# Performance work log

Hardware: AMD Instinct MI355X
Metric: run time of the kernel (lower is better)

The kernel has to match this reference:

```python
import jax, jax.numpy as jnp
import numpy as np

D = 4096        # hidden_dim / latent_dim
R = 512         # number of latents
H = 32          # n_heads
HD = D // H     # head_dim = 128
T = 8192        # total tokens (sum of seqlens)
EPS = 1e-5


def layernorm(x, w, b):
    mu = jnp.mean(x, axis=-1, keepdims=True)
    var = jnp.mean(jnp.square(x - mu), axis=-1, keepdims=True)
    return (x - mu) * jax.lax.rsqrt(var + EPS) * w + b


def setup_inputs() -> dict:
    key = jax.random.key(0)
    ks = jax.random.split(key, 16)
    s = 0.02
    inp = {
        'x': jax.random.normal(ks[0], (T, D), jnp.float32),
        'seqlens': jnp.full((8,), T // 8, jnp.int64) if False else jnp.full((8,), T // 8, jnp.int32),
        'latents': jax.random.normal(ks[1], (R, D), jnp.float32),
        # PreNorm layernorms (query norm on x, context norm on latents)
        'ln_q_w': 1.0 + 0.1 * jax.random.normal(ks[2], (D,), jnp.float32),
        'ln_q_b': 0.1 * jax.random.normal(ks[3], (D,), jnp.float32),
        'ln_c_w': 1.0 + 0.1 * jax.random.normal(ks[4], (D,), jnp.float32),
        'ln_c_b': 0.1 * jax.random.normal(ks[5], (D,), jnp.float32),
        # attention projections, stored (in, out) so y = x @ W
        'Wq': s * jax.random.normal(ks[6], (D, D), jnp.float32),
        'Wk': s * jax.random.normal(ks[7], (D, D), jnp.float32),
        'Wv': s * jax.random.normal(ks[8], (D, D), jnp.float32),
        'Wo': s * jax.random.normal(ks[9], (D, D), jnp.float32),
        # single PreNorm MLP block (n_layers=1)
        'ln_m_w': 1.0 + 0.1 * jax.random.normal(ks[10], (D,), jnp.float32),
        'ln_m_b': 0.1 * jax.random.normal(ks[11], (D,), jnp.float32),
        'W1': s * jax.random.normal(ks[12], (D, D), jnp.float32),
        'W2': s * jax.random.normal(ks[13], (D, D), jnp.float32),
    }
    return inp


def reference(x, seqlens, latents, ln_q_w, ln_q_b, ln_c_w, ln_c_b,
              Wq, Wk, Wv, Wo, ln_m_w, ln_m_b, W1, W2):
    # --- PreNorm cross-attention: queries = ragged tokens, KV = latents ---
    # BlockDiagonalMask(q_seqlen=seqlens, kv_seqlen=[r]*b) with identical
    # latents per block == dense attention of all tokens vs the r latents.
    xq = layernorm(x, ln_q_w, ln_q_b)                 # (T, D)
    xc = layernorm(latents, ln_c_w, ln_c_b)           # (R, D)
    q = (xq @ Wq).reshape(T, H, HD)                   # (T, H, HD)
    k = (xc @ Wk).reshape(R, H, HD)                   # (R, H, HD)
    v = (xc @ Wv).reshape(R, H, HD)
    scale = HD ** -0.5
    scores = jnp.einsum('thd,rhd->htr', q, k) * scale  # (H, T, R)
    attn = jax.nn.softmax(scores, axis=-1)
    o = jnp.einsum('htr,rhd->thd', attn, v).reshape(T, D)
    attn_out = o @ Wo                                  # (T, D)

    hiddens = attn_out + x                             # residual

    # --- PreNorm MLP block (n_layers=1) ---
    y = layernorm(hiddens, ln_m_w, ln_m_b)
    m = jax.nn.gelu(y @ W1, approximate=False) @ W2 + y  # MLP_block inner residual
    hiddens = m + hiddens                                # outer residual

    # compress_rate == -1 -> mean_mask is None, output passes through
    return hiddens
```

## Files before the change

### kernel.cpp

```cpp
#include <hip/hip_runtime.h>
#include <hip/hip_bf16.h>
#include <math.h>

#define D 4096
#define T 8192
#define R 512
#define HD 128
#define NH 32

typedef unsigned short u16;
typedef u16 u16x8 __attribute__((ext_vector_type(8)));
typedef __bf16 bf16x8 __attribute__((ext_vector_type(8)));
typedef float f32x4 __attribute__((ext_vector_type(4)));

__device__ __forceinline__ u16 f2bf(float f) {
  unsigned u = __builtin_bit_cast(unsigned, f);
  u += 0x7FFFu + ((u >> 16) & 1u);
  return (u16)(u >> 16);
}
__device__ __forceinline__ float bf2f(u16 b) {
  return __builtin_bit_cast(float, ((unsigned)b) << 16);
}
__device__ __forceinline__ bf16x8 ldb8(const u16* p) {
  return __builtin_bit_cast(bf16x8, *(const u16x8*)p);
}
__device__ __forceinline__ void async_cp16(void* gsrc, void* ldst) {
  typedef __attribute__((address_space(1))) void gvoid;
  typedef __attribute__((address_space(3))) void lvoid;
  __builtin_amdgcn_global_load_lds((gvoid*)gsrc, (lvoid*)ldst, 16, 0, 0);
}
#define MFMA(a, b, c) __builtin_amdgcn_mfma_f32_16x16x32_bf16(a, b, c, 0, 0, 0)

__global__ __launch_bounds__(256) void ln_bf16(
    const float* __restrict__ X, const float* __restrict__ w,
    const float* __restrict__ b, u16* __restrict__ out) {
  const int row = blockIdx.x, tid = threadIdx.x;
  const int lane = tid & 63, wv = tid >> 6;
  const float* xr = X + (long)row * D;
  float4 v[4];
  float s = 0.f, ss = 0.f;
#pragma unroll
  for (int i = 0; i < 4; ++i) {
    v[i] = *(const float4*)(xr + tid * 4 + i * 1024);
    s += v[i].x + v[i].y + v[i].z + v[i].w;
    ss += v[i].x * v[i].x + v[i].y * v[i].y + v[i].z * v[i].z + v[i].w * v[i].w;
  }
#pragma unroll
  for (int off = 32; off >= 1; off >>= 1) {
    s += __shfl_xor(s, off);
    ss += __shfl_xor(ss, off);
  }
  __shared__ float sw[4], ssw[4];
  if (lane == 0) { sw[wv] = s; ssw[wv] = ss; }
  __syncthreads();
  s = sw[0] + sw[1] + sw[2] + sw[3];
  ss = ssw[0] + ssw[1] + ssw[2] + ssw[3];
  const float mu = s * (1.f / D);
  const float var = ss * (1.f / D) - mu * mu;
  const float rstd = rsqrtf(var + 1e-5f);
#pragma unroll
  for (int i = 0; i < 4; ++i) {
    const int base = tid * 4 + i * 1024;
    const float4 wv4 = *(const float4*)(w + base);
    const float4 bv4 = *(const float4*)(b + base);
    ushort4 ov;
    ov.x = f2bf((v[i].x - mu) * rstd * wv4.x + bv4.x);
    ov.y = f2bf((v[i].y - mu) * rstd * wv4.y + bv4.y);
    ov.z = f2bf((v[i].z - mu) * rstd * wv4.z + bv4.z);
    ov.w = f2bf((v[i].w - mu) * rstd * wv4.w + bv4.w);
    *(ushort4*)(out + (long)row * D + base) = ov;
  }
}

__global__ __launch_bounds__(256) void wconv(const float* __restrict__ W,
                                             u16* __restrict__ Wt) {
  __shared__ float t[32][33];
  const int tx = threadIdx.x & 31, ty = threadIdx.x >> 5;
  const int n0 = blockIdx.x * 32, k0 = blockIdx.y * 32;
#pragma unroll
  for (int i = 0; i < 4; ++i)
    t[ty + i * 8][tx] = W[(long)(k0 + ty + i * 8) * D + n0 + tx];
  __syncthreads();
#pragma unroll
  for (int i = 0; i < 4; ++i)
    Wt[(long)(n0 + ty + i * 8) * D + k0 + tx] = f2bf(t[tx][ty + i * 8]);
}

template <int EPI>
__global__ __launch_bounds__(256) void gemm_bt(
    const u16* __restrict__ A, const u16* __restrict__ Bt, u16* __restrict__ ob,
    u16* __restrict__ ob2, float* __restrict__ of, const float* __restrict__ af,
    const u16* __restrict__ ab, float scale) {
  __shared__ u16 As[128 * 32];
  __shared__ u16 Bs[128 * 32];
  const int tid = threadIdx.x;
  const int bx = blockIdx.x, by = blockIdx.y;
  const int lane = tid & 63, w = tid >> 6;
  const int ln15 = lane & 15, q = lane >> 4;
  const int wm = (w >> 1) * 64, wn = (w & 1) * 64;

  const int c0 = tid, c1 = tid + 256;
  const u16* ag0 = A + (long)(by * 128 + (c0 >> 2)) * D + (c0 & 3) * 8;
  const u16* ag1 = A + (long)(by * 128 + (c1 >> 2)) * D + (c1 & 3) * 8;
  const u16* bg0 = Bt + (long)(bx * 128 + (c0 >> 2)) * D + (c0 & 3) * 8;
  const u16* bg1 = Bt + (long)(bx * 128 + (c1 >> 2)) * D + (c1 & 3) * 8;
  u16* al0 = As + (tid & ~63) * 8;
  u16* al1 = As + ((tid & ~63) + 256) * 8;
  u16* bl0 = Bs + (tid & ~63) * 8;
  u16* bl1 = Bs + ((tid & ~63) + 256) * 8;

  f32x4 acc[4][4];
#pragma unroll
  for (int i = 0; i < 4; ++i)
#pragma unroll
    for (int j = 0; j < 4; ++j) {
      f32x4 z = {0.f, 0.f, 0.f, 0.f};
      acc[i][j] = z;
    }

  for (int k0 = 0; k0 < D; k0 += 32) {
    __syncthreads();
    async_cp16((void*)(ag0 + k0), al0);
    async_cp16((void*)(ag1 + k0), al1);
    async_cp16((void*)(bg0 + k0), bl0);
    async_cp16((void*)(bg1 + k0), bl1);
    __syncthreads();
    bf16x8 av[4], bv[4];
#pragma unroll
    for (int i = 0; i < 4; ++i) av[i] = ldb8(As + (wm + i * 16 + ln15) * 32 + q * 8);
#pragma unroll
    for (int j = 0; j < 4; ++j) bv[j] = ldb8(Bs + (wn + j * 16 + ln15) * 32 + q * 8);
#pragma unroll
    for (int i = 0; i < 4; ++i)
#pragma unroll
      for (int j = 0; j < 4; ++j) acc[i][j] = MFMA(av[i], bv[j], acc[i][j]);
  }

#pragma unroll
  for (int i = 0; i < 4; ++i) {
    const int gmb = by * 128 + wm + i * 16 + q * 4;
#pragma unroll
    for (int j = 0; j < 4; ++j) {
      const int gn = bx * 128 + wn + j * 16 + ln15;
#pragma unroll
      for (int r = 0; r < 4; ++r) {
        const int gm = gmb + r;
        const float vacc = acc[i][j][r];
        const long idx = (long)gm * D + gn;
        if constexpr (EPI == 0) {
          ob[idx] = f2bf(vacc * scale);
        } else if constexpr (EPI == 1) {
          if (gn < D)
            ob[idx] = f2bf(vacc);
          else
            ob2[(long)(gn - D) * R + gm] = f2bf(vacc);
        } else if constexpr (EPI == 2) {
          of[idx] = vacc + af[idx];
        } else if constexpr (EPI == 3) {
          ob[idx] = f2bf(0.5f * vacc * (1.f + erff(vacc * 0.7071067811865475f)));
        } else {
          of[idx] = of[idx] + vacc + bf2f(ab[idx]);
        }
      }
    }
  }
}

__global__ __launch_bounds__(256) void attn_fused(const u16* Q,
                                                  const u16* __restrict__ Kb,
                                                  const u16* __restrict__ Vt,
                                                  u16* O) {
  __shared__ u16 Qs[64 * 136];
  __shared__ u16 Ks[64 * 136];
  __shared__ u16 Vs[128 * 72];
  __shared__ u16 Ps[4][16 * 72];
  const int tid = threadIdx.x;
  const int lane = tid & 63, w = tid >> 6;
  const int ln15 = lane & 15, q = lane >> 4;
  const int t0 = blockIdx.x * 64, h = blockIdx.y;

#pragma unroll
  for (int it = 0; it < 4; ++it) {
    const int c = tid + it * 256;
    const int row = c >> 4, cj = c & 15;
    *(u16x8*)(Qs + row * 136 + cj * 8) =
        *(const u16x8*)(Q + (long)(t0 + row) * D + h * HD + cj * 8);
  }

  f32x4 o[8];
  float m_run[4], l_run[4];
#pragma unroll
  for (int t = 0; t < 8; ++t) {
    f32x4 z = {0.f, 0.f, 0.f, 0.f};
    o[t] = z;
  }
#pragma unroll
  for (int r = 0; r < 4; ++r) {
    m_run[r] = -1e30f;
    l_run[r] = 0.f;
  }

  for (int ch = 0; ch < 8; ++ch) {
    const int r0 = ch * 64;
    __syncthreads();
#pragma unroll
    for (int it = 0; it < 4; ++it) {
      const int c = tid + it * 256;
      const int row = c >> 4, cj = c & 15;
      *(u16x8*)(Ks + row * 136 + cj * 8) =
          *(const u16x8*)(Kb + (long)(r0 + row) * D + h * HD + cj * 8);
    }
#pragma unroll
    for (int it = 0; it < 4; ++it) {
      const int c = tid + it * 256;
      const int hd = c >> 3, rj = c & 7;
      *(u16x8*)(Vs + hd * 72 + rj * 8) =
          *(const u16x8*)(Vt + (long)(h * HD + hd) * R + r0 + rj * 8);
    }
    __syncthreads();

    f32x4 s[4];
#pragma unroll
    for (int j = 0; j < 4; ++j) {
      f32x4 z = {0.f, 0.f, 0.f, 0.f};
      s[j] = z;
    }
#pragma unroll
    for (int kk = 0; kk < 4; ++kk) {
      const bf16x8 a = ldb8(Qs + (w * 16 + ln15) * 136 + kk * 32 + q * 8);
#pragma unroll
      for (int j = 0; j < 4; ++j) {
        const bf16x8 b = ldb8(Ks + (j * 16 + ln15) * 136 + kk * 32 + q * 8);
        s[j] = MFMA(a, b, s[j]);
      }
    }
    float mx[4], rs[4];
#pragma unroll
    for (int r = 0; r < 4; ++r)
      mx[r] = fmaxf(fmaxf(s[0][r], s[1][r]), fmaxf(s[2][r], s[3][r]));
#pragma unroll
    for (int off = 8; off >= 1; off >>= 1)
#pragma unroll
      for (int r = 0; r < 4; ++r) mx[r] = fmaxf(mx[r], __shfl_xor(mx[r], off));
#pragma unroll
    for (int r = 0; r < 4; ++r) {
      const float mn = fmaxf(m_run[r], mx[r]);
      const float al = __expf(m_run[r] - mn);
      m_run[r] = mn;
      float a2 = 0.f;
#pragma unroll
      for (int j = 0; j < 4; ++j) {
        const float p = __expf(s[j][r] - mn);
        s[j][r] = p;
        a2 += p;
      }
      rs[r] = a2;
      l_run[r] *= al;
#pragma unroll
      for (int t = 0; t < 8; ++t) o[t][r] *= al;
    }
#pragma unroll
    for (int off = 8; off >= 1; off >>= 1)
#pragma unroll
      for (int r = 0; r < 4; ++r) rs[r] += __shfl_xor(rs[r], off);
#pragma unroll
    for (int r = 0; r < 4; ++r) l_run[r] += rs[r];
#pragma unroll
    for (int j = 0; j < 4; ++j)
#pragma unroll
      for (int r = 0; r < 4; ++r)
        Ps[w][(q * 4 + r) * 72 + j * 16 + ln15] = f2bf(s[j][r]);
    __syncthreads();
#pragma unroll
    for (int kk = 0; kk < 2; ++kk) {
      const bf16x8 a = ldb8(Ps[w] + ln15 * 72 + kk * 32 + q * 8);
#pragma unroll
      for (int t = 0; t < 8; ++t) {
        const bf16x8 b = ldb8(Vs + (t * 16 + ln15) * 72 + kk * 32 + q * 8);
        o[t] = MFMA(a, b, o[t]);
      }
    }
  }
#pragma unroll
  for (int r = 0; r < 4; ++r) l_run[r] = 1.f / l_run[r];
#pragma unroll
  for (int t = 0; t < 8; ++t)
#pragma unroll
    for (int r = 0; r < 4; ++r) {
      const int row = t0 + w * 16 + q * 4 + r;
      const int col = h * HD + t * 16 + ln15;
      O[(long)row * D + col] = f2bf(o[t][r] * l_run[r]);
    }
}

extern "C" void kernel_launch(void* const* d_in, const int* in_sizes, int n_in,
                              void* d_out, int out_size, void* d_ws, size_t ws_size,
                              hipStream_t stream) {
  (void)in_sizes; (void)n_in; (void)out_size;
  const float* x      = (const float*)d_in[0];
  const float* lat    = (const float*)d_in[2];
  const float* ln_q_w = (const float*)d_in[3];
  const float* ln_q_b = (const float*)d_in[4];
  const float* ln_c_w = (const float*)d_in[5];
  const float* ln_c_b = (const float*)d_in[6];
  const float* Wq     = (const float*)d_in[7];
  const float* Wk     = (const float*)d_in[8];
  const float* Wv     = (const float*)d_in[9];
  const float* Wo     = (const float*)d_in[10];
  const float* ln_m_w = (const float*)d_in[11];
  const float* ln_m_b = (const float*)d_in[12];
  const float* W1     = (const float*)d_in[13];
  const float* W2     = (const float*)d_in[14];
  float* out = (float*)d_out;

  const long DD = (long)D * D, TD = (long)T * D, RD = (long)R * D;
  u16* p = (u16*)d_ws;
  u16* Wt   = p; p += 2 * DD;
  u16* a_bf = p; p += TD;
  u16* q_bf = p; p += TD;
  u16* xc   = p; p += RD;
  u16* k_bf = p; p += RD;
  u16* v_t  = p; p += RD;
  if (ws_size < (size_t)(p - (u16*)d_ws) * sizeof(u16)) return;

  const dim3 B(256);
  const dim3 Gw(128, 128);
  const dim3 Gg(32, 64);

  ln_bf16<<<T, B, 0, stream>>>(x, ln_q_w, ln_q_b, a_bf);
  ln_bf16<<<R, B, 0, stream>>>(lat, ln_c_w, ln_c_b, xc);

  wconv<<<Gw, B, 0, stream>>>(Wq, Wt);
  gemm_bt<0><<<Gg, B, 0, stream>>>(a_bf, Wt, q_bf, nullptr, nullptr, nullptr,
                                   nullptr, 0.08838834764831845f);

  wconv<<<Gw, B, 0, stream>>>(Wk, Wt);
  wconv<<<Gw, B, 0, stream>>>(Wv, Wt + DD);
  gemm_bt<1><<<dim3(64, 4), B, 0, stream>>>(xc, Wt, k_bf, v_t, nullptr, nullptr,
                                            nullptr, 1.f);

  attn_fused<<<dim3(128, 32), B, 0, stream>>>(q_bf, k_bf, v_t, q_bf);

  wconv<<<Gw, B, 0, stream>>>(Wo, Wt);
  gemm_bt<2><<<Gg, B, 0, stream>>>(q_bf, Wt, nullptr, nullptr, out, x, nullptr, 1.f);

  ln_bf16<<<T, B, 0, stream>>>(out, ln_m_w, ln_m_b, a_bf);

  wconv<<<Gw, B, 0, stream>>>(W1, Wt);
  gemm_bt<3><<<Gg, B, 0, stream>>>(a_bf, Wt, q_bf, nullptr, nullptr, nullptr,
                                   nullptr, 1.f);

  wconv<<<Gw, B, 0, stream>>>(W2, Wt);
  gemm_bt<4><<<Gg, B, 0, stream>>>(q_bf, Wt, nullptr, nullptr, out, nullptr,
                                   a_bf, 1.f);
}
```

Measured before the change: 2.266 ms.

## Replace 128x128 GEMMs with 256x256-tile 512-thread pipelined bf16 GEMM

Adds a new gemm256 kernel that uses 256x256 output tiles, 8 waves per block and double-buffered LDS filled with async global-to-LDS copies into XOR-swizzled layouts. The kernel interleaves LDS fragment reads and next-tile prefetch with MFMA groups, separated by barriers and raised wave priority. The four large DxD projections (Wq, Wo, W1, W2) now use it in place of the 128x128 gemm_bt. The goal is more data reuse per loaded byte and better overlap of memory with matrix math. The cost is higher register and LDS pressure, more barriers per k-step, and a 512-block grid that may fill the GPU unevenly.

Result: faster. 1.986 ms (-12.4%).

```diff
diff --git a/kernel.cpp b/kernel.cpp
--- a/kernel.cpp
+++ b/kernel.cpp
@@ -30,6 +30,12 @@
   __builtin_amdgcn_global_load_lds((gvoid*)gsrc, (lvoid*)ldst, 16, 0, 0);
 }
 #define MFMA(a, b, c) __builtin_amdgcn_mfma_f32_16x16x32_bf16(a, b, c, 0, 0, 0)
+
+__device__ __forceinline__ void wg_barrier() {
+  asm volatile("" ::: "memory");
+  __builtin_amdgcn_s_barrier();
+  asm volatile("" ::: "memory");
+}
 
 __global__ __launch_bounds__(256) void ln_bf16(
     const float* __restrict__ X, const float* __restrict__ w,
@@ -147,13 +153,160 @@
         const int gm = gmb + r;
         const float vacc = acc[i][j][r];
         const long idx = (long)gm * D + gn;
-        if constexpr (EPI == 0) {
-          ob[idx] = f2bf(vacc * scale);
-        } else if constexpr (EPI == 1) {
+        if constexpr (EPI == 1) {
           if (gn < D)
             ob[idx] = f2bf(vacc);
           else
             ob2[(long)(gn - D) * R + gm] = f2bf(vacc);
+        } else {
+          ob[idx] = f2bf(vacc * scale);
+        }
+      }
+    }
+  }
+}
+
+template <int MG>
+__device__ __forceinline__ void readA(bf16x8 (&bA)[2][4], const u16* aB,
+                                      int base, int cc0, int cc1) {
+#pragma unroll
+  for (int im = 0; im < 4; ++im) {
+    bA[0][im] = ldb8(aB + (MG * 4 + im) * 1024 + base + cc0);
+    bA[1][im] = ldb8(aB + (MG * 4 + im) * 1024 + base + cc1);
+  }
+}
+template <int NJ0>
+__device__ __forceinline__ void readB(bf16x8 (&bB)[2][4], const u16* bP,
+                                      int base, int cc0, int cc1) {
+#pragma unroll
+  for (int nj = 0; nj < 2; ++nj) {
+    bB[0][NJ0 + nj] = ldb8(bP + (NJ0 + nj) * 1024 + base + cc0);
+    bB[1][NJ0 + nj] = ldb8(bP + (NJ0 + nj) * 1024 + base + cc1);
+  }
+}
+template <int MG, int NJ0>
+__device__ __forceinline__ void mfma16(f32x4 (&acc)[8][4], const bf16x8 (&bA)[2][4],
+                                       const bf16x8 (&bB)[2][4]) {
+#pragma unroll
+  for (int im = 0; im < 4; ++im)
+#pragma unroll
+    for (int nj = 0; nj < 2; ++nj)
+#pragma unroll
+      for (int kk = 0; kk < 2; ++kk)
+        acc[MG * 4 + im][NJ0 + nj] =
+            MFMA(bA[kk][im], bB[kk][NJ0 + nj], acc[MG * 4 + im][NJ0 + nj]);
+}
+
+template <int EPI>
+__global__ __launch_bounds__(512, 2) void gemm256(
+    const u16* __restrict__ A, const u16* __restrict__ Bt, u16* __restrict__ ob,
+    float* __restrict__ of, const float* __restrict__ af,
+    const u16* __restrict__ ab, float scale) {
+  __shared__ u16 As[2][2][8192];
+  __shared__ u16 Bs[2][2][8192];
+  const int tid = threadIdx.x;
+  const int bx = blockIdx.x, by = blockIdx.y;
+  const int lane = tid & 63, w = tid >> 6;
+  const int ln15 = lane & 15, q = lane >> 4;
+  const int wm = w >> 2, wn = w & 3;
+
+  const int r0 = tid >> 3, s0 = (tid & 7) ^ (r0 & 7);
+  const int r1 = 64 + r0, s1 = (tid & 7) ^ (r1 & 7);
+  const long oA00 = (long)(by * 256 + r0) * D + s0 * 8;
+  const long oA01 = (long)(by * 256 + r1) * D + s1 * 8;
+  const long oA10 = (long)(by * 256 + 128 + r0) * D + s0 * 8;
+  const long oA11 = (long)(by * 256 + 128 + r1) * D + s1 * 8;
+  const long oB00 = (long)(bx * 256 + r0) * D + s0 * 8;
+  const long oB01 = (long)(bx * 256 + r1) * D + s1 * 8;
+  const long oB10 = (long)(bx * 256 + 128 + r0) * D + s0 * 8;
+  const long oB11 = (long)(bx * 256 + 128 + r1) * D + s1 * 8;
+  const int d0 = w * 512, d1 = 4096 + w * 512;
+
+  const int sw = ln15 & 7;
+  const int cc0 = (q ^ sw) * 8;
+  const int cc1 = ((4 + q) ^ sw) * 8;
+  const int baseA = ln15 * 64;
+  const int baseB = (wn & 1) * 4096 + ln15 * 64;
+
+  f32x4 acc[8][4];
+#pragma unroll
+  for (int i = 0; i < 8; ++i)
+#pragma unroll
+    for (int j = 0; j < 4; ++j) {
+      f32x4 z = {0.f, 0.f, 0.f, 0.f};
+      acc[i][j] = z;
+    }
+
+  auto stageA = [&](int buf, int kt) {
+    async_cp16((void*)(A + oA00 + kt * 64), &As[buf][0][d0]);
+    async_cp16((void*)(A + oA01 + kt * 64), &As[buf][0][d1]);
+    async_cp16((void*)(A + oA10 + kt * 64), &As[buf][1][d0]);
+    async_cp16((void*)(A + oA11 + kt * 64), &As[buf][1][d1]);
+  };
+  auto stageB = [&](int buf, int kt) {
+    async_cp16((void*)(Bt + oB00 + kt * 64), &Bs[buf][0][d0]);
+    async_cp16((void*)(Bt + oB01 + kt * 64), &Bs[buf][0][d1]);
+    async_cp16((void*)(Bt + oB10 + kt * 64), &Bs[buf][1][d0]);
+    async_cp16((void*)(Bt + oB11 + kt * 64), &Bs[buf][1][d1]);
+  };
+
+  stageA(0, 0);
+  stageB(0, 0);
+  asm volatile("s_waitcnt vmcnt(0)" ::: "memory");
+  wg_barrier();
+
+  int cur = 0;
+  for (int t = 0; t < D / 64; ++t) {
+    const int nxt = cur ^ 1;
+    const bool pf = (t + 1 < D / 64);
+    const u16* aB = &As[cur][wm][0];
+    const u16* bP = &Bs[cur][wn >> 1][0];
+    bf16x8 bA[2][4], bB[2][4];
+    readA<0>(bA, aB, baseA, cc0, cc1);
+    readB<0>(bB, bP, baseB, cc0, cc1);
+    if (pf) stageA(nxt, t + 1);
+    wg_barrier();
+    asm volatile("s_waitcnt lgkmcnt(0)" ::: "memory");
+    __builtin_amdgcn_s_setprio(1);
+    mfma16<0, 0>(acc, bA, bB);
+    __builtin_amdgcn_s_setprio(0);
+    wg_barrier();
+    readB<2>(bB, bP, baseB, cc0, cc1);
+    if (pf) stageB(nxt, t + 1);
+    wg_barrier();
+    asm volatile("s_waitcnt lgkmcnt(0)" ::: "memory");
+    __builtin_amdgcn_s_setprio(1);
+    mfma16<0, 2>(acc, bA, bB);
+    __builtin_amdgcn_s_setprio(0);
+    wg_barrier();
+    readA<1>(bA, aB, baseA, cc0, cc1);
+    wg_barrier();
+    asm volatile("s_waitcnt lgkmcnt(0)" ::: "memory");
+    __builtin_amdgcn_s_setprio(1);
+    mfma16<1, 0>(acc, bA, bB);
+    __builtin_amdgcn_s_setprio(0);
+    wg_barrier();
+    __builtin_amdgcn_s_setprio(1);
+    mfma16<1, 2>(acc, bA, bB);
+    __builtin_amdgcn_s_setprio(0);
+    asm volatile("s_waitcnt vmcnt(0)" ::: "memory");
+    wg_barrier();
+    cur = nxt;
+  }
+
+#pragma unroll
+  for (int mi = 0; mi < 8; ++mi) {
+    const int gmb = by * 256 + wm * 128 + mi * 16 + q * 4;
+#pragma unroll
+    for (int nj = 0; nj < 4; ++nj) {
+      const int gn = bx * 256 + wn * 64 + nj * 16 + ln15;
+#pragma unroll
+      for (int r = 0; r < 4; ++r) {
+        const int gm = gmb + r;
+        const float vacc = acc[mi][nj][r];
+        const long idx = (long)gm * D + gn;
+        if constexpr (EPI == 0) {
+          ob[idx] = f2bf(vacc * scale);
         } else if constexpr (EPI == 2) {
           of[idx] = vacc + af[idx];
         } else if constexpr (EPI == 3) {
@@ -324,15 +477,16 @@
   if (ws_size < (size_t)(p - (u16*)d_ws) * sizeof(u16)) return;
 
   const dim3 B(256);
+  const dim3 B5(512);
   const dim3 Gw(128, 128);
-  const dim3 Gg(32, 64);
+  const dim3 Gg(16, 32);
 
   ln_bf16<<<T, B, 0, stream>>>(x, ln_q_w, ln_q_b, a_bf);
   ln_bf16<<<R, B, 0, stream>>>(lat, ln_c_w, ln_c_b, xc);
 
   wconv<<<Gw, B, 0, stream>>>(Wq, Wt);
-  gemm_bt<0><<<Gg, B, 0, stream>>>(a_bf, Wt, q_bf, nullptr, nullptr, nullptr,
-                                   nullptr, 0.08838834764831845f);
+  gemm256<0><<<Gg, B5, 0, stream>>>(a_bf, Wt, q_bf, nullptr, nullptr, nullptr,
+                                    0.08838834764831845f);
 
   wconv<<<Gw, B, 0, stream>>>(Wk, Wt);
   wconv<<<Gw, B, 0, stream>>>(Wv, Wt + DD);
@@ -342,15 +496,13 @@
   attn_fused<<<dim3(128, 32), B, 0, stream>>>(q_bf, k_bf, v_t, q_bf);
 
   wconv<<<Gw, B, 0, stream>>>(Wo, Wt);
-  gemm_bt<2><<<Gg, B, 0, stream>>>(q_bf, Wt, nullptr, nullptr, out, x, nullptr, 1.f);
+  gemm256<2><<<Gg, B5, 0, stream>>>(q_bf, Wt, nullptr, out, x, nullptr, 1.f);
 
   ln_bf16<<<T, B, 0, stream>>>(out, ln_m_w, ln_m_b, a_bf);
 
   wconv<<<Gw, B, 0, stream>>>(W1, Wt);
-  gemm_bt<3><<<Gg, B, 0, stream>>>(a_bf, Wt, q_bf, nullptr, nullptr, nullptr,
-                                   nullptr, 1.f);
+  gemm256<3><<<Gg, B5, 0, stream>>>(a_bf, Wt, q_bf, nullptr, nullptr, nullptr, 1.f);
 
   wconv<<<Gw, B, 0, stream>>>(W2, Wt);
-  gemm_bt<4><<<Gg, B, 0, stream>>>(q_bf, Wt, nullptr, nullptr, out, nullptr,
-                                   a_bf, 1.f);
-}
+  gemm256<4><<<Gg, B5, 0, stream>>>(q_bf, Wt, nullptr, out, nullptr, a_bf, 1.f);
+}
```
